# Optimization experiments

Measured on AMD Instinct MI355X. Metric: run time of the kernel, lower is better.

The kernel has to match this reference:

```python
import jax, jax.numpy as jnp
import numpy as np
import math

B, C, H, W = 16, 256, 128, 128
IC = 32  # inter_channels = in_channels // r


def setup_inputs() -> dict:
    key = jax.random.key(0)
    ks = jax.random.split(key, 7)
    s_in = 1.0 / math.sqrt(C)   # ~ conv kaiming-uniform scale for C->IC 1x1 conv
    s_out = 1.0 / math.sqrt(IC)  # for IC->C 1x1 conv
    return {
        "x": jax.random.normal(ks[0], (B, C, H, W), dtype=jnp.float32),
        "g_w": jax.random.normal(ks[1], (IC, C), dtype=jnp.float32) * s_in,
        "g_b": jax.random.normal(ks[2], (IC,), dtype=jnp.float32) * s_in,
        "theta_w": jax.random.normal(ks[3], (IC, C), dtype=jnp.float32) * s_in,
        "theta_b": jax.random.normal(ks[4], (IC,), dtype=jnp.float32) * s_in,
        "w_w": jax.random.normal(ks[5], (C, IC), dtype=jnp.float32) * s_out,
        "w_b": jax.random.normal(ks[6], (C,), dtype=jnp.float32) * s_out,
    }


def reference(x, g_w, g_b, theta_w, theta_b, w_w, w_b):
    b, c, h, w = x.shape
    m = h * w
    ic = g_w.shape[0]
    xf = x.reshape(b, c, m)  # (B, C, M)
    # 1x1 convs == per-pixel channel matmuls
    g_x = jnp.einsum('ic,bcm->bim', g_w, xf) + g_b[None, :, None]      # (B, IC, M)
    t = jnp.einsum('ic,bcm->bim', theta_w, xf) + theta_b[None, :, None]  # (B, IC, M)
    # sigma = theta_x_T @ I_hat @ theta_x with I_hat = I/M - 11^T/M^2
    #       = (t t^T)/M - mu mu^T  (closed form; avoids (M,M) matrix)
    mu = jnp.mean(t, axis=-1)  # (B, IC)
    sigma = jnp.einsum('bim,bjm->bij', t, t) / m - mu[:, :, None] * mu[:, None, :]
    sigma = sigma / math.sqrt(ic)
    attn = jax.nn.softmax(sigma, axis=-1)  # (B, IC, IC)
    y = jnp.einsum('bij,bjm->bim', attn, g_x)  # (B, IC, M)
    w_y = jnp.einsum('ci,bim->bcm', w_w, y) + w_b[None, :, None]  # (B, C, M)
    return (w_y + xf).reshape(b, c, h, w)
```

## Files before the change

### kernel.cpp

```cpp
#include <hip/hip_runtime.h>
#include <math.h>

constexpr int Bn  = 16;
constexpr int Cn  = 256;
constexpr int Mn  = 16384;
constexpr int ICn = 32;

constexpr size_t OFF_GX  = 0;
constexpr size_t OFF_WT  = OFF_GX  + (size_t)Bn * ICn * Mn;
constexpr size_t OFF_WCT = OFF_WT  + (size_t)Cn * 64;
constexpr size_t OFF_TT  = OFF_WCT + (size_t)Bn * ICn * Cn;
constexpr size_t OFF_MU  = OFF_TT  + (size_t)Bn * ICn * ICn;

__global__ void k0_transpose_w(const float* __restrict__ g_w,
                               const float* __restrict__ theta_w,
                               float* __restrict__ wt) {
    int idx = blockIdx.x * 256 + threadIdx.x;
    int k = idx >> 6;
    int i = idx & 63;
    float v = (i < 32) ? g_w[i * Cn + k] : theta_w[(i - 32) * Cn + k];
    wt[idx] = v;
}

__global__ __launch_bounds__(256, 4) void k1_proj(
    const float* __restrict__ x,
    const float* __restrict__ wt,
    const float* __restrict__ g_b,
    const float* __restrict__ theta_b,
    float* __restrict__ gx,
    float* __restrict__ tt,
    float* __restrict__ mu)
{
    __shared__ float ts[32][260];
    __shared__ float sig[ICn * ICn];

    const int tx = threadIdx.x;
    const int b  = blockIdx.y;
    const int m0 = blockIdx.x * 256;
    const int mq = tx & 63;
    const int ig = tx >> 6;
    const int igu = __builtin_amdgcn_readfirstlane(ig);
    const int m  = m0 + mq * 4;

    for (int p = tx; p < ICn * ICn; p += 256) sig[p] = 0.f;

    float acc[16][4];
    #pragma unroll
    for (int i = 0; i < 16; ++i)
        acc[i][0] = acc[i][1] = acc[i][2] = acc[i][3] = 0.f;

    const float4* __restrict__ xq =
        (const float4*)(x + (size_t)b * Cn * Mn + m);
    const float* __restrict__ wtg = wt + igu * 16;

    #pragma unroll 4
    for (int k = 0; k < Cn; ++k) {
        float4 xv = xq[(size_t)k * (Mn / 4)];
        #pragma unroll
        for (int i = 0; i < 16; ++i) {
            float w = wtg[k * 64 + i];
            acc[i][0] += w * xv.x;
            acc[i][1] += w * xv.y;
            acc[i][2] += w * xv.z;
            acc[i][3] += w * xv.w;
        }
    }

    if (ig < 2) {
        #pragma unroll
        for (int i = 0; i < 16; ++i) {
            int gi = ig * 16 + i;
            float bb = g_b[gi];
            float4 v = make_float4(acc[i][0] + bb, acc[i][1] + bb,
                                   acc[i][2] + bb, acc[i][3] + bb);
            *(float4*)(gx + ((size_t)b * ICn + gi) * Mn + m) = v;
        }
    } else {
        #pragma unroll
        for (int i = 0; i < 16; ++i) {
            int ti = (ig - 2) * 16 + i;
            float bb = theta_b[ti];
            float4 v = make_float4(acc[i][0] + bb, acc[i][1] + bb,
                                   acc[i][2] + bb, acc[i][3] + bb);
            *(float4*)&ts[ti][mq * 4] = v;
        }
    }
    __syncthreads();

    {
        const int i0 = (tx & 7) * 4;
        const int j0 = ((tx >> 3) & 7) * 4;
        const int ms = (tx >> 6) * 64;
        float s2[4][4] = {};
        for (int mm = 0; mm < 64; mm += 4) {
            float4 av[4], bv[4];
            #pragma unroll
            for (int a = 0; a < 4; ++a) av[a] = *(const float4*)&ts[i0 + a][ms + mm];
            #pragma unroll
            for (int c = 0; c < 4; ++c) bv[c] = *(const float4*)&ts[j0 + c][ms + mm];
            #pragma unroll
            for (int a = 0; a < 4; ++a)
                #pragma unroll
                for (int c = 0; c < 4; ++c)
                    s2[a][c] += av[a].x * bv[c].x + av[a].y * bv[c].y +
                                av[a].z * bv[c].z + av[a].w * bv[c].w;
        }
        #pragma unroll
        for (int a = 0; a < 4; ++a)
            #pragma unroll
            for (int c = 0; c < 4; ++c)
                atomicAdd(&sig[(i0 + a) * 32 + (j0 + c)], s2[a][c]);
    }

    {
        int i = tx & 31, seg = tx >> 5;
        const float* r = &ts[i][seg * 32];
        float s = 0.f;
        #pragma unroll
        for (int q = 0; q < 32; q += 4) {
            float4 v = *(const float4*)(r + q);
            s += (v.x + v.y) + (v.z + v.w);
        }
        atomicAdd(&mu[b * ICn + i], s);
    }

    __syncthreads();
    for (int p = tx; p < ICn * ICn; p += 256)
        atomicAdd(&tt[b * ICn * ICn + p], sig[p]);
}

__global__ void k2_attn(const float* __restrict__ tt,
                        const float* __restrict__ mu_in,
                        const float* __restrict__ w_w,
                        float* __restrict__ wct)
{
    __shared__ float s_mu[ICn];
    __shared__ float s_sig[ICn][ICn];
    __shared__ float s_attn[ICn][ICn];
    const int b  = blockIdx.x;
    const int tx = threadIdx.x;

    if (tx < ICn) s_mu[tx] = mu_in[b * ICn + tx] * (1.f / Mn);
    __syncthreads();

    for (int p = tx; p < ICn * ICn; p += 256) {
        int i = p >> 5, j = p & 31;
        s_sig[i][j] = (tt[b * ICn * ICn + p] * (1.f / Mn) - s_mu[i] * s_mu[j])
                      * 0.17677669529663687f;
    }
    __syncthreads();

    if (tx < ICn) {
        float mx = -1e30f;
        #pragma unroll
        for (int j = 0; j < ICn; ++j) mx = fmaxf(mx, s_sig[tx][j]);
        float e[ICn];
        float sum = 0.f;
        #pragma unroll
        for (int j = 0; j < ICn; ++j) { e[j] = __expf(s_sig[tx][j] - mx); sum += e[j]; }
        float r = 1.f / sum;
        #pragma unroll
        for (int j = 0; j < ICn; ++j) s_attn[tx][j] = e[j] * r;
    }
    __syncthreads();

    const int c = tx;
    float wr[ICn];
    #pragma unroll
    for (int i = 0; i < ICn; i += 4) {
        float4 v = *(const float4*)(w_w + c * ICn + i);
        wr[i] = v.x; wr[i + 1] = v.y; wr[i + 2] = v.z; wr[i + 3] = v.w;
    }
    for (int j = 0; j < ICn; ++j) {
        float s = 0.f;
        #pragma unroll
        for (int i = 0; i < ICn; ++i) s += wr[i] * s_attn[i][j];
        wct[((size_t)b * ICn + j) * Cn + c] = s;
    }
}

__global__ __launch_bounds__(256, 4) void k3_out(
    const float* __restrict__ x,
    const float* __restrict__ gx,
    const float* __restrict__ wct,
    const float* __restrict__ w_b,
    float* __restrict__ out)
{
    __shared__ float wc_s[ICn][Cn];
    __shared__ float gx_s[ICn][64];
    __shared__ float wb_s[Cn];

    const int tx = threadIdx.x;
    const int b  = blockIdx.y;
    const int m0 = blockIdx.x * 64;

    {
        const float4* src = (const float4*)(wct + (size_t)b * ICn * Cn);
        float4* dst = (float4*)wc_s;
        #pragma unroll
        for (int p = tx; p < ICn * Cn / 4; p += 256) dst[p] = src[p];
    }
    {
        int r  = tx >> 3;
        int c8 = (tx & 7) * 8;
        const float* g = gx + ((size_t)b * ICn + r) * Mn + m0 + c8;
        *(float4*)&gx_s[r][c8]     = *(const float4*)g;
        *(float4*)&gx_s[r][c8 + 4] = *(const float4*)(g + 4);
    }
    if (tx < 64) ((float4*)wb_s)[tx] = ((const float4*)w_b)[tx];
    __syncthreads();

    const int mg = tx & 15;
    const int cg = tx >> 4;
    float acc[16][4] = {};

    #pragma unroll
    for (int j = 0; j < ICn; ++j) {
        float4 g4 = *(const float4*)&gx_s[j][mg * 4];
        #pragma unroll
        for (int cc = 0; cc < 16; ++cc) {
            float w = wc_s[j][cg * 16 + cc];
            acc[cc][0] += w * g4.x;
            acc[cc][1] += w * g4.y;
            acc[cc][2] += w * g4.z;
            acc[cc][3] += w * g4.w;
        }
    }

    const size_t mbase = (size_t)b * Cn * Mn + m0 + mg * 4;
    #pragma unroll
    for (int cc = 0; cc < 16; ++cc) {
        int c = cg * 16 + cc;
        float4 xv = *(const float4*)(x + mbase + (size_t)c * Mn);
        float wb = wb_s[c];
        float4 o;
        o.x = acc[cc][0] + xv.x + wb;
        o.y = acc[cc][1] + xv.y + wb;
        o.z = acc[cc][2] + xv.z + wb;
        o.w = acc[cc][3] + xv.w + wb;
        *(float4*)(out + mbase + (size_t)c * Mn) = o;
    }
}

extern "C" void kernel_launch(void* const* d_in, const int* in_sizes, int n_in,
                              void* d_out, int out_size, void* d_ws, size_t ws_size,
                              hipStream_t stream) {
    const float* x    = (const float*)d_in[0];
    const float* g_w  = (const float*)d_in[1];
    const float* g_b  = (const float*)d_in[2];
    const float* th_w = (const float*)d_in[3];
    const float* th_b = (const float*)d_in[4];
    const float* w_w  = (const float*)d_in[5];
    const float* w_b  = (const float*)d_in[6];
    float* out = (float*)d_out;
    float* ws  = (float*)d_ws;

    float* gx  = ws + OFF_GX;
    float* wt  = ws + OFF_WT;
    float* wct = ws + OFF_WCT;
    float* tt  = ws + OFF_TT;
    float* mu  = ws + OFF_MU;

    hipMemsetAsync(tt, 0, (size_t)(Bn * ICn * ICn + Bn * ICn) * sizeof(float), stream);

    k0_transpose_w<<<64, 256, 0, stream>>>(g_w, th_w, wt);
    k1_proj<<<dim3(64, Bn), 256, 0, stream>>>(x, wt, g_b, th_b, gx, tt, mu);
    k2_attn<<<Bn, 256, 0, stream>>>(tt, mu, w_w, wct);
    k3_out<<<dim3(Mn / 64, Bn), 256, 0, stream>>>(x, gx, wct, w_b, out);
}
```

Measured before the change: 608.4 us.

## Rewrite projection kernel with bf16 MFMA and swizzled shared weights

The fp32 FMA projection kernel is replaced by one that converts x and the packed g/theta weights to bf16 and computes the C->64 projections with 16x16x32 bf16 MFMA instructions. Weights are pre-swizzled into a bf16 buffer and staged in LDS to avoid bank conflicts, and the theta Gram matrix is also computed with MFMA on bf16 tiles. Tiles shrink to 64 pixels, giving four times as many blocks, with atomics straight to global tt. This targets the compute-bound fp32 projection but lowers precision to bf16 and adds more global atomics.

```diff
diff --git a/kernel.cpp b/kernel.cpp
--- a/kernel.cpp
+++ b/kernel.cpp
@@ -6,127 +6,132 @@
 constexpr int Mn  = 16384;
 constexpr int ICn = 32;
 
+typedef float v4f   __attribute__((ext_vector_type(4)));
+typedef short short8 __attribute__((ext_vector_type(8)));
+
 constexpr size_t OFF_GX  = 0;
-constexpr size_t OFF_WT  = OFF_GX  + (size_t)Bn * ICn * Mn;
-constexpr size_t OFF_WCT = OFF_WT  + (size_t)Cn * 64;
+constexpr size_t OFF_WBF = OFF_GX  + (size_t)Bn * ICn * Mn;
+constexpr size_t OFF_WCT = OFF_WBF + 8192;
 constexpr size_t OFF_TT  = OFF_WCT + (size_t)Bn * ICn * Cn;
 constexpr size_t OFF_MU  = OFF_TT  + (size_t)Bn * ICn * ICn;
 
-__global__ void k0_transpose_w(const float* __restrict__ g_w,
-                               const float* __restrict__ theta_w,
-                               float* __restrict__ wt) {
+__device__ inline unsigned short f2bf(float f) {
+    unsigned u = __float_as_uint(f);
+    u += 0x7fffu + ((u >> 16) & 1u);
+    return (unsigned short)(u >> 16);
+}
+
+__global__ void k0_prep_w(const float* __restrict__ g_w,
+                          const float* __restrict__ th_w,
+                          unsigned short* __restrict__ wbf) {
     int idx = blockIdx.x * 256 + threadIdx.x;
-    int k = idx >> 6;
-    int i = idx & 63;
-    float v = (i < 32) ? g_w[i * Cn + k] : theta_w[(i - 32) * Cn + k];
-    wt[idx] = v;
-}
-
-__global__ __launch_bounds__(256, 4) void k1_proj(
+    int row = idx >> 8, ks = idx & 255;
+    int slot = ks >> 3;
+    int k = ((slot ^ (row & 7)) << 3) | (ks & 7);
+    float v = (row < ICn) ? g_w[row * Cn + k] : th_w[(row - ICn) * Cn + k];
+    wbf[idx] = f2bf(v);
+}
+
+__global__ __launch_bounds__(256, 4) void k1_mfma(
     const float* __restrict__ x,
-    const float* __restrict__ wt,
+    const unsigned short* __restrict__ wbf,
     const float* __restrict__ g_b,
     const float* __restrict__ theta_b,
     float* __restrict__ gx,
     float* __restrict__ tt,
     float* __restrict__ mu)
 {
-    __shared__ float ts[32][260];
-    __shared__ float sig[ICn * ICn];
-
-    const int tx = threadIdx.x;
-    const int b  = blockIdx.y;
-    const int m0 = blockIdx.x * 256;
-    const int mq = tx & 63;
-    const int ig = tx >> 6;
-    const int igu = __builtin_amdgcn_readfirstlane(ig);
-    const int m  = m0 + mq * 4;
-
-    for (int p = tx; p < ICn * ICn; p += 256) sig[p] = 0.f;
-
-    float acc[16][4];
-    #pragma unroll
-    for (int i = 0; i < 16; ++i)
-        acc[i][0] = acc[i][1] = acc[i][2] = acc[i][3] = 0.f;
-
-    const float4* __restrict__ xq =
-        (const float4*)(x + (size_t)b * Cn * Mn + m);
-    const float* __restrict__ wtg = wt + igu * 16;
-
-    #pragma unroll 4
-    for (int k = 0; k < Cn; ++k) {
-        float4 xv = xq[(size_t)k * (Mn / 4)];
-        #pragma unroll
-        for (int i = 0; i < 16; ++i) {
-            float w = wtg[k * 64 + i];
-            acc[i][0] += w * xv.x;
-            acc[i][1] += w * xv.y;
-            acc[i][2] += w * xv.z;
-            acc[i][3] += w * xv.w;
-        }
-    }
-
-    if (ig < 2) {
-        #pragma unroll
-        for (int i = 0; i < 16; ++i) {
-            int gi = ig * 16 + i;
-            float bb = g_b[gi];
-            float4 v = make_float4(acc[i][0] + bb, acc[i][1] + bb,
-                                   acc[i][2] + bb, acc[i][3] + bb);
-            *(float4*)(gx + ((size_t)b * ICn + gi) * Mn + m) = v;
-        }
-    } else {
-        #pragma unroll
-        for (int i = 0; i < 16; ++i) {
-            int ti = (ig - 2) * 16 + i;
-            float bb = theta_b[ti];
-            float4 v = make_float4(acc[i][0] + bb, acc[i][1] + bb,
-                                   acc[i][2] + bb, acc[i][3] + bb);
-            *(float4*)&ts[ti][mq * 4] = v;
-        }
-    }
-    __syncthreads();
-
-    {
-        const int i0 = (tx & 7) * 4;
-        const int j0 = ((tx >> 3) & 7) * 4;
-        const int ms = (tx >> 6) * 64;
-        float s2[4][4] = {};
-        for (int mm = 0; mm < 64; mm += 4) {
-            float4 av[4], bv[4];
+    __shared__ __align__(16) unsigned short Ws[64 * 256];
+    __shared__ __align__(16) unsigned short Ts[32 * 72];
+    __shared__ float mu_s[ICn];
+
+    const int tx   = threadIdx.x;
+    const int b    = blockIdx.y;
+    const int m0   = blockIdx.x * 64;
+    const int lane = tx & 63;
+    const int w    = tx >> 6;
+    const int ln15 = lane & 15;
+    const int q    = lane >> 4;
+
+    {
+        const int4* src = (const int4*)wbf;
+        int4* dst = (int4*)Ws;
+        #pragma unroll
+        for (int i = 0; i < 8; ++i) dst[tx + 256 * i] = src[tx + 256 * i];
+    }
+    if (tx < ICn) mu_s[tx] = 0.f;
+    __syncthreads();
+
+    v4f acc[4];
+    #pragma unroll
+    for (int nt = 0; nt < 4; ++nt) acc[nt] = (v4f){0.f, 0.f, 0.f, 0.f};
+
+    const float* xbase = x + ((size_t)b * Cn + q * 8) * Mn + m0 + w * 16 + ln15;
+
+    float xf[8];
+    #pragma unroll
+    for (int j = 0; j < 8; ++j) xf[j] = xbase[(size_t)j * Mn];
+
+    #pragma unroll
+    for (int kc = 0; kc < 8; ++kc) {
+        short8 a;
+        #pragma unroll
+        for (int j = 0; j < 8; ++j) a[j] = (short)f2bf(xf[j]);
+        if (kc < 7) {
             #pragma unroll
-            for (int a = 0; a < 4; ++a) av[a] = *(const float4*)&ts[i0 + a][ms + mm];
-            #pragma unroll
-            for (int c = 0; c < 4; ++c) bv[c] = *(const float4*)&ts[j0 + c][ms + mm];
-            #pragma unroll
-            for (int a = 0; a < 4; ++a)
-                #pragma unroll
-                for (int c = 0; c < 4; ++c)
-                    s2[a][c] += av[a].x * bv[c].x + av[a].y * bv[c].y +
-                                av[a].z * bv[c].z + av[a].w * bv[c].w;
-        }
-        #pragma unroll
-        for (int a = 0; a < 4; ++a)
-            #pragma unroll
-            for (int c = 0; c < 4; ++c)
-                atomicAdd(&sig[(i0 + a) * 32 + (j0 + c)], s2[a][c]);
-    }
-
-    {
-        int i = tx & 31, seg = tx >> 5;
-        const float* r = &ts[i][seg * 32];
+            for (int j = 0; j < 8; ++j)
+                xf[j] = xbase[(size_t)((kc + 1) * 32 + j) * Mn];
+        }
+        #pragma unroll
+        for (int nt = 0; nt < 4; ++nt) {
+            int row  = nt * 16 + ln15;
+            int slot = (kc * 4 + q) ^ (row & 7);
+            short8 bf = *(const short8*)&Ws[row * 256 + slot * 8];
+            acc[nt] = __builtin_amdgcn_mfma_f32_16x16x32_bf16(a, bf, acc[nt], 0, 0, 0);
+        }
+    }
+
+    #pragma unroll
+    for (int nt = 0; nt < 2; ++nt) {
+        int row = nt * 16 + ln15;
+        float bb = g_b[row];
+        float* gp = gx + ((size_t)b * ICn + row) * Mn + m0 + w * 16 + q * 4;
+        #pragma unroll
+        for (int r = 0; r < 4; ++r) gp[r] = acc[nt][r] + bb;
+    }
+
+    #pragma unroll
+    for (int nt = 2; nt < 4; ++nt) {
+        int tr = (nt - 2) * 16 + ln15;
+        float bb = theta_b[tr];
         float s = 0.f;
         #pragma unroll
-        for (int q = 0; q < 32; q += 4) {
-            float4 v = *(const float4*)(r + q);
-            s += (v.x + v.y) + (v.z + v.w);
-        }
-        atomicAdd(&mu[b * ICn + i], s);
-    }
-
-    __syncthreads();
-    for (int p = tx; p < ICn * ICn; p += 256)
-        atomicAdd(&tt[b * ICn * ICn + p], sig[p]);
+        for (int r = 0; r < 4; ++r) {
+            float tv = acc[nt][r] + bb;
+            Ts[tr * 72 + w * 16 + q * 4 + r] = f2bf(tv);
+            s += tv;
+        }
+        s += __shfl_xor(s, 16);
+        s += __shfl_xor(s, 32);
+        if (q == 0) atomicAdd(&mu_s[tr], s);
+    }
+    __syncthreads();
+
+    {
+        int i0 = (w & 1) * 16, j0 = (w >> 1) * 16;
+        v4f at = (v4f){0.f, 0.f, 0.f, 0.f};
+        #pragma unroll
+        for (int pc = 0; pc < 2; ++pc) {
+            short8 A  = *(const short8*)&Ts[(i0 + ln15) * 72 + pc * 32 + q * 8];
+            short8 Bv = *(const short8*)&Ts[(j0 + ln15) * 72 + pc * 32 + q * 8];
+            at = __builtin_amdgcn_mfma_f32_16x16x32_bf16(A, Bv, at, 0, 0, 0);
+        }
+        float* ttb = tt + (size_t)b * ICn * ICn;
+        #pragma unroll
+        for (int r = 0; r < 4; ++r)
+            atomicAdd(&ttb[(i0 + q * 4 + r) * ICn + j0 + ln15], at[r]);
+    }
+    if (tx < ICn) atomicAdd(&mu[b * ICn + tx], mu_s[tx]);
 }
 
 __global__ void k2_attn(const float* __restrict__ tt,
@@ -255,16 +260,16 @@
     float* out = (float*)d_out;
     float* ws  = (float*)d_ws;
 
-    float* gx  = ws + OFF_GX;
-    float* wt  = ws + OFF_WT;
-    float* wct = ws + OFF_WCT;
-    float* tt  = ws + OFF_TT;
-    float* mu  = ws + OFF_MU;
+    float* gx            = ws + OFF_GX;
+    unsigned short* wbf  = (unsigned short*)(ws + OFF_WBF);
+    float* wct           = ws + OFF_WCT;
+    float* tt            = ws + OFF_TT;
+    float* mu            = ws + OFF_MU;
 
     hipMemsetAsync(tt, 0, (size_t)(Bn * ICn * ICn + Bn * ICn) * sizeof(float), stream);
 
-    k0_transpose_w<<<64, 256, 0, stream>>>(g_w, th_w, wt);
-    k1_proj<<<dim3(64, Bn), 256, 0, stream>>>(x, wt, g_b, th_b, gx, tt, mu);
+    k0_prep_w<<<64, 256, 0, stream>>>(g_w, th_w, wbf);
+    k1_mfma<<<dim3(Mn / 64, Bn), 256, 0, stream>>>(x, wbf, g_b, th_b, gx, tt, mu);
     k2_attn<<<Bn, 256, 0, stream>>>(tt, mu, w_w, wct);
     k3_out<<<dim3(Mn / 64, Bn), 256, 0, stream>>>(x, gx, wct, w_b, out);
 }
```

Result: faster. 560.6 us (-7.9%).
